# Kernel tuning notes

Measured on AMD Instinct MI355X. Metric: run time of the kernel, lower is better.

Reference implementation:

```python
import jax, jax.numpy as jnp
import numpy as np

B, N, D, H = 2, 192, 256, 8
DH = D // H
SCALE = 1.0 / float(np.sqrt(DH))


def setup_inputs() -> dict:
    key = jax.random.key(0)
    ks = jax.random.split(key, 20)
    def w(k, shape, s=0.02):
        return jax.random.normal(k, shape, dtype=jnp.float32) * s
    inp = {}
    inp['x'] = jax.random.normal(ks[0], (B, N, D), dtype=jnp.float32)
    inp['e'] = jax.random.normal(ks[1], (B, N, N, D), dtype=jnp.float32)
    for name in ['ln_x', 'ln_e', 'ln_x2', 'ln_e2']:
        inp[name + '_g'] = jnp.ones((D,), jnp.float32)
        inp[name + '_b'] = jnp.zeros((D,), jnp.float32)
    # per-head stacked projection weights: [H, D, DH]
    for i, n in enumerate(['Wq_en', 'Wk_en', 'Wv_en', 'Wq_ne', 'Wk_ne', 'Wv_ne']):
        inp[n] = w(ks[2 + i], (H, D, DH))
        inp['b' + n[1:]] = jnp.zeros((H, DH), jnp.float32)
    inp['WOx_w'] = w(ks[10], (D, D)); inp['WOx_b'] = jnp.zeros((D,), jnp.float32)
    inp['WOe_w'] = w(ks[11], (D, D)); inp['WOe_b'] = jnp.zeros((D,), jnp.float32)
    inp['mlpx_w1'] = w(ks[12], (4 * D, D)); inp['mlpx_b1'] = jnp.zeros((4 * D,), jnp.float32)
    inp['mlpx_w2'] = w(ks[13], (D, 4 * D)); inp['mlpx_b2'] = jnp.zeros((D,), jnp.float32)
    inp['mlpe_w1'] = w(ks[14], (4 * D, D)); inp['mlpe_b1'] = jnp.zeros((4 * D,), jnp.float32)
    inp['mlpe_w2'] = w(ks[15], (D, 4 * D)); inp['mlpe_b2'] = jnp.zeros((D,), jnp.float32)
    return inp


def layer_norm(v, g, b, eps=1e-5):
    m = jnp.mean(v, axis=-1, keepdims=True)
    var = jnp.mean((v - m) ** 2, axis=-1, keepdims=True)
    return (v - m) * jax.lax.rsqrt(var + eps) * g + b


def reference(x, e, ln_x_g, ln_x_b, ln_e_g, ln_e_b, ln_x2_g, ln_x2_b, ln_e2_g, ln_e2_b,
              Wq_en, bq_en, Wk_en, bk_en, Wv_en, bv_en,
              Wq_ne, bq_ne, Wk_ne, bk_ne, Wv_ne, bv_ne,
              WOx_w, WOx_b, WOe_w, WOe_b,
              mlpx_w1, mlpx_b1, mlpx_w2, mlpx_b2,
              mlpe_w1, mlpe_b1, mlpe_w2, mlpe_b2):
    b_, n_, d_ = x.shape
    xn = layer_norm(x, ln_x_g, ln_x_b)
    en = layer_norm(e, ln_e_g, ln_e_b)

    # --- edge-to-node cross attention (node i attends over its edges (i, j)) ---
    Q = jnp.einsum('bnd,hde->bnhe', xn, Wq_en) + bq_en          # [B,N,H,DH]
    K = jnp.einsum('bijd,hde->bijhe', en, Wk_en) + bk_en        # [B,N,N,H,DH]
    V = jnp.einsum('bijd,hde->bijhe', en, Wv_en) + bv_en
    s = jnp.einsum('bihe,bijhe->bijh', Q, K) * SCALE            # [B,N,N,H]
    a = jax.nn.softmax(s, axis=2)
    x_heads = jnp.einsum('bijh,bijhe->bihe', a, V)              # [B,N,H,DH]
    x_mha = x_heads.reshape(b_, n_, d_) @ WOx_w.T + WOx_b

    # --- node-to-edge cross attention (edge (i,j) attends over endpoints i, j) ---
    Qe = jnp.einsum('bijd,hde->bijhe', en, Wq_ne) + bq_ne       # [B,N,N,H,DH]
    Kx = jnp.einsum('bnd,hde->bnhe', xn, Wk_ne) + bk_ne         # [B,N,H,DH]
    Vx = jnp.einsum('bnd,hde->bnhe', xn, Wv_ne) + bv_ne
    si = jnp.einsum('bijhe,bihe->bijh', Qe, Kx) * SCALE
    sj = jnp.einsum('bijhe,bjhe->bijh', Qe, Kx) * SCALE
    m = jnp.maximum(si, sj)
    ei = jnp.exp(si - m)
    ej = jnp.exp(sj - m)
    den = ei + ej
    ai = (ei / den)[..., None]                                   # [B,N,N,H,1]
    aj = (ej / den)[..., None]
    e_heads = ai * Vx[:, :, None] + aj * Vx[:, None, :]          # [B,N,N,H,DH]
    e_mha = e_heads.reshape(b_, n_, n_, d_) @ WOe_w.T + WOe_b

    # --- residuals + MLPs ---
    x_out = xn + x_mha
    hx = layer_norm(x_out, ln_x2_g, ln_x2_b)
    hx = jax.nn.leaky_relu(hx @ mlpx_w1.T + mlpx_b1, 0.01) @ mlpx_w2.T + mlpx_b2
    x_out = x_out + hx

    e_out = en + e_mha
    he = layer_norm(e_out, ln_e2_g, ln_e2_b)
    he = jax.nn.leaky_relu(he @ mlpe_w1.T + mlpe_b1, 0.01) @ mlpe_w2.T + mlpe_b2
    e_out = e_out + he
    return (x_out, e_out)
```

## Files before the change

kernel.cpp:

```cpp
#include <hip/hip_runtime.h>
#include <hip/hip_bf16.h>
#include <math.h>

#define BB 2
#define NN 192
#define DD 256
#define HH 8
#define DHH 32
#define SCALE 0.17677669529663687f
#define SJ 4
#define NS6 6
#define NTILE (BB * NN * 6)

typedef __attribute__((ext_vector_type(8))) short short8;
typedef __attribute__((ext_vector_type(4))) float f32x4;


__device__ __forceinline__ float red32(float v) {
    v += __shfl_xor(v, 16);
    v += __shfl_xor(v, 8);
    v += __shfl_xor(v, 4);
    v += __shfl_xor(v, 2);
    v += __shfl_xor(v, 1);
    return v;
}

__device__ __forceinline__ unsigned short f2bf(float f) {
    unsigned int u = __builtin_bit_cast(unsigned int, f);
    u += 0x7FFFu + ((u >> 16) & 1u);
    return (unsigned short)(u >> 16);
}

__device__ __forceinline__ float bf2f(unsigned short u) {
    unsigned int v = ((unsigned int)u) << 16;
    return __builtin_bit_cast(float, v);
}

__device__ __forceinline__ void ln8(float (*xs)[DD], const float* __restrict__ g,
                                    const float* __restrict__ b,
                                    float* mred, float* rred) {
    int t = threadIdx.x;
    int r = t >> 5, l = t & 31;
    float s = 0.f, s2 = 0.f;
#pragma unroll
    for (int u = 0; u < 8; u++) {
        float v = xs[r][l + 32 * u];
        s += v; s2 += v * v;
    }
    s = red32(s); s2 = red32(s2);
    if (l == 0) {
        float mean = s * (1.f / 256.f);
        float var  = s2 * (1.f / 256.f) - mean * mean;
        mred[r] = mean;
        rred[r] = rsqrtf(var + 1e-5f);
    }
    __syncthreads();
    float gt = g[t], bt = b[t];
#pragma unroll
    for (int rr = 0; rr < 8; rr++) {
        float v = xs[rr][t];
        xs[rr][t] = (v - mred[rr]) * rred[rr] * gt + bt;
    }
    __syncthreads();
}

__device__ __forceinline__ void gemm256f8(const unsigned short (*A)[264],
                                          const unsigned short* __restrict__ Wf,
                                          int w, int lane, int fr, int fq,
                                          f32x4 acc[2][2]) {
#pragma unroll
    for (int m = 0; m < 2; m++)
#pragma unroll
        for (int nt = 0; nt < 2; nt++) acc[m][nt] = (f32x4){0.f, 0.f, 0.f, 0.f};
    short8 nb[2];
#pragma unroll
    for (int nt = 0; nt < 2; nt++)
        nb[nt] = *(const short8*)(Wf + (((size_t)(w * 2 + nt) * 8 + 0) * 64 + lane) * 8);
#pragma unroll
    for (int k = 0; k < 8; k++) {
        short8 cb[2];
#pragma unroll
        for (int nt = 0; nt < 2; nt++) cb[nt] = nb[nt];
        if (k < 7) {
#pragma unroll
            for (int nt = 0; nt < 2; nt++)
                nb[nt] = *(const short8*)(Wf + (((size_t)(w * 2 + nt) * 8 + k + 1) * 64 + lane) * 8);
        }
        short8 a0 = *(const short8*)&A[fr][k * 32 + fq * 8];
        short8 a1 = *(const short8*)&A[16 + fr][k * 32 + fq * 8];
#pragma unroll
        for (int nt = 0; nt < 2; nt++) {
            acc[0][nt] = __builtin_amdgcn_mfma_f32_16x16x32_bf16(a0, cb[nt], acc[0][nt], 0, 0, 0);
            acc[1][nt] = __builtin_amdgcn_mfma_f32_16x16x32_bf16(a1, cb[nt], acc[1][nt], 0, 0, 0);
        }
    }
}

__global__ void k_node_prep(const float* __restrict__ x,
                            const float* __restrict__ lnxg, const float* __restrict__ lnxb,
                            const float* __restrict__ Wq, const float* __restrict__ bq,
                            const float* __restrict__ Wk, const float* __restrict__ bk,
                            const float* __restrict__ Wv, const float* __restrict__ bv,
                            float* __restrict__ xn, float* __restrict__ Qb,
                            float* __restrict__ Kx, float* __restrict__ Vx) {
    __shared__ float xs[8][DD];
    __shared__ float mred[8], rred[8];
    int t = threadIdx.x;
    int r0 = blockIdx.x * 8;
    for (int r = 0; r < 8; r++) xs[r][t] = x[(r0 + r) * DD + t];
    __syncthreads();
    ln8(xs, lnxg, lnxb, mred, rred);
    for (int r = 0; r < 8; r++) xn[(r0 + r) * DD + t] = xs[r][t];
    int h = t >> 5, d_ = t & 31;
    const float* wq = Wq + h * DD * DHH + d_;
    const float* wk = Wk + h * DD * DHH + d_;
    const float* wv = Wv + h * DD * DHH + d_;
    float aq[8] = {0}, ak[8] = {0}, av[8] = {0};
    for (int k = 0; k < DD; k++) {
        float w1 = wq[k * DHH], w2 = wk[k * DHH], w3 = wv[k * DHH];
#pragma unroll
        for (int r = 0; r < 8; r++) {
            float e = xs[r][k];
            aq[r] += e * w1; ak[r] += e * w2; av[r] += e * w3;
        }
    }
    float bqt = bq[t], bkt = bk[t], bvt = bv[t];
    for (int r = 0; r < 8; r++) {
        Qb[(r0 + r) * DD + t] = aq[r] + bqt;
        Kx[(r0 + r) * DD + t] = ak[r] + bkt;
        Vx[(r0 + r) * DD + t] = av[r] + bvt;
    }
}

__global__ void k_cvt_all(const float* __restrict__ w1, const float* __restrict__ w2,
                          const float* __restrict__ WOe,
                          const float* __restrict__ Wq, const float* __restrict__ Wk,
                          const float* __restrict__ Wv,
                          unsigned short* __restrict__ w1f, unsigned short* __restrict__ w2f,
                          unsigned short* __restrict__ WOef,
                          unsigned short* __restrict__ Wqf, unsigned short* __restrict__ Wkf,
                          unsigned short* __restrict__ Wvf) {
    int bid = blockIdx.x, t = threadIdx.x;
    short8 out;
    if (bid < 128) {
        int fi = bid * 256 + t;
        int l = fi & 63, g = fi >> 6;
        int fr = l & 15, fq = l >> 4;
        int tau = g >> 3, kap = g & 7;
        const float* src = w1 + (size_t)(tau * 16 + fr) * 256 + kap * 32 + fq * 8;
#pragma unroll
        for (int u = 0; u < 8; u++) out[u] = (short)f2bf(src[u]);
        *(short8*)(w1f + (size_t)fi * 8) = out;
    } else if (bid < 256) {
        int fi = (bid - 128) * 256 + t;
        int l = fi & 63, g = fi >> 6;
        int fr = l & 15, fq = l >> 4;
        int tau = g >> 5, kap = g & 31;
        const float* src = w2 + (size_t)(tau * 16 + fr) * 1024 + kap * 32 + fq * 8;
#pragma unroll
        for (int u = 0; u < 8; u++) out[u] = (short)f2bf(src[u]);
        *(short8*)(w2f + (size_t)fi * 8) = out;
    } else if (bid < 288) {
        int fi = (bid - 256) * 256 + t;
        int l = fi & 63, g = fi >> 6;
        int fr = l & 15, fq = l >> 4;
        int tau = g >> 3, kap = g & 7;
        const float* src = WOe + (size_t)(tau * 16 + fr) * 256 + kap * 32 + fq * 8;
#pragma unroll
        for (int u = 0; u < 8; u++) out[u] = (short)f2bf(src[u]);
        *(short8*)(WOef + (size_t)fi * 8) = out;
    } else {
        int which = (bid - 288) >> 5;
        int fi = ((bid - 288) & 31) * 256 + t;
        int l = fi & 63, g = fi >> 6;
        int fr = l & 15, fq = l >> 4;
        int tau = g >> 3, kap = g & 7;
        int n = tau * 16 + fr;
        int k0 = kap * 32 + fq * 8;
        const float* src = which == 0 ? Wq : which == 1 ? Wk : Wv;
        const float* s2 = src + (size_t)(n >> 5) * 8192 + (n & 31);
#pragma unroll
        for (int u = 0; u < 8; u++) out[u] = (short)f2bf(s2[(size_t)(k0 + u) * 32]);
        unsigned short* dst = which == 0 ? Wqf : which == 1 ? Wkf : Wvf;
        *(short8*)(dst + (size_t)fi * 8) = out;
    }
}

__global__ __launch_bounds__(512, 2) void k_n2e_fused(
    const float* __restrict__ e,
    const float* __restrict__ lneg, const float* __restrict__ lneb,
    const unsigned short* __restrict__ Wqf, const float* __restrict__ bq,
    const unsigned short* __restrict__ Wkf, const float* __restrict__ bk,
    const unsigned short* __restrict__ Wvf, const float* __restrict__ bv,
    const float* __restrict__ Kx, const float* __restrict__ Vx,
    const float* __restrict__ Qb,
    const unsigned short* __restrict__ WOef, const float* __restrict__ WOb,
    const float* __restrict__ ln2g, const float* __restrict__ ln2b,
    const unsigned short* __restrict__ w1f, const float* __restrict__ b1,
    const unsigned short* __restrict__ w2f, const float* __restrict__ b2,
    float* __restrict__ oute,
    float* __restrict__ accP6, float* __restrict__ mP6, float* __restrict__ lP6) {
    __shared__ unsigned short a_bf[32][264];
    __shared__ unsigned short p_bf[32][264];
    __shared__ float KxiS[DD], VxiS[DD], QbS[DD];
    __shared__ float mrow[32], rrow[32];
    __shared__ float sW[32][8], s2W[32][8];
    __shared__ float m2s[32], r2s[32];
    int t = threadIdx.x, lane = t & 63, w = t >> 6;
    int fr = lane & 15, fq = lane >> 4;
    int blk = blockIdx.x;
    int b   = blk / (NN * 6);
    int rem = blk % (NN * 6);
    int i   = rem / 6;
    int spl = rem % 6;
    int j0  = spl * 32;
    int node = b * NN + i;
    size_t ebase = ((size_t)node * NN + j0) * DD;

    {
        int r = t >> 4, sub = t & 15;
        const float4* src4 = (const float4*)(e + ebase + (size_t)r * DD + sub * 16);
        float vals[16];
        float s = 0.f, s2 = 0.f;
#pragma unroll
        for (int u = 0; u < 4; u++) {
            float4 v = src4[u];
            vals[4 * u + 0] = v.x; vals[4 * u + 1] = v.y;
            vals[4 * u + 2] = v.z; vals[4 * u + 3] = v.w;
            s += v.x + v.y + v.z + v.w;
            s2 += v.x * v.x + v.y * v.y + v.z * v.z + v.w * v.w;
        }
        s += __shfl_xor(s, 8); s2 += __shfl_xor(s2, 8);
        s += __shfl_xor(s, 4); s2 += __shfl_xor(s2, 4);
        s += __shfl_xor(s, 2); s2 += __shfl_xor(s2, 2);
        s += __shfl_xor(s, 1); s2 += __shfl_xor(s2, 1);
        float mean = s * (1.f / 256.f);
        float rstd = rsqrtf(s2 * (1.f / 256.f) - mean * mean + 1e-5f);
        if (sub == 0) { mrow[r] = mean; rrow[r] = rstd; }
#pragma unroll
        for (int u = 0; u < 16; u += 2) {
            int col = sub * 16 + u;
            float n0 = (vals[u]     - mean) * rstd * lneg[col]     + lneb[col];
            float n1 = (vals[u + 1] - mean) * rstd * lneg[col + 1] + lneb[col + 1];
            unsigned int pk = (unsigned int)f2bf(n0) | ((unsigned int)f2bf(n1) << 16);
            *(unsigned int*)&a_bf[r][col] = pk;
        }
    }
    if (t < DD) {
        KxiS[t] = Kx[node * DD + t];
        VxiS[t] = Vx[node * DD + t];
        QbS[t]  = Qb[node * DD + t];
    }
    __syncthreads();

    const int nw = w * 32;

    f32x4 accQ[2][2];
    gemm256f8(a_bf, Wqf, w, lane, fr, fq, accQ);
    {
        float bqv[2];
#pragma unroll
        for (int nt = 0; nt < 2; nt++) bqv[nt] = bq[nw + nt * 16 + fr];
#pragma unroll
        for (int m = 0; m < 2; m++)
#pragma unroll
            for (int nt = 0; nt < 2; nt++)
#pragma unroll
                for (int j = 0; j < 4; j++) accQ[m][nt][j] += bqv[nt];
    }

    f32x4 accK[2][2];
    gemm256f8(a_bf, Wkf, w, lane, fr, fq, accK);
#pragma unroll
    for (int nt = 0; nt < 2; nt++) {
        float bb = bk[nw + nt * 16 + fr];
#pragma unroll
        for (int m = 0; m < 2; m++)
#pragma unroll
            for (int j = 0; j < 4; j++) accK[m][nt][j] += bb;
    }

    f32x4 accV[2][2];
    gemm256f8(a_bf, Wvf, w, lane, fr, fq, accV);
#pragma unroll
    for (int nt = 0; nt < 2; nt++) {
        float bb = bv[nw + nt * 16 + fr];
#pragma unroll
        for (int m = 0; m < 2; m++)
#pragma unroll
            for (int j = 0; j < 4; j++) accV[m][nt][j] += bb;
    }

    {
        float QbL[2];
        QbL[0] = QbS[nw + fr];
        QbL[1] = QbS[nw + 16 + fr];
        float p[2][4];
        float mx = -1e30f;
#pragma unroll
        for (int m = 0; m < 2; m++)
#pragma unroll
            for (int j = 0; j < 4; j++) {
                float s = accK[m][0][j] * QbL[0] + accK[m][1][j] * QbL[1];
                s += __shfl_xor(s, 1);
                s += __shfl_xor(s, 2);
                s += __shfl_xor(s, 4);
                s += __shfl_xor(s, 8);
                s *= SCALE;
                p[m][j] = s;
                mx = fmaxf(mx, s);
            }
        mx = fmaxf(mx, __shfl_xor(mx, 16));
        mx = fmaxf(mx, __shfl_xor(mx, 32));
        float lsum = 0.f;
#pragma unroll
        for (int m = 0; m < 2; m++)
#pragma unroll
            for (int j = 0; j < 4; j++) {
                p[m][j] = __expf(p[m][j] - mx);
                lsum += p[m][j];
            }
        lsum += __shfl_xor(lsum, 16);
        lsum += __shfl_xor(lsum, 32);
        float part[2];
#pragma unroll
        for (int nt = 0; nt < 2; nt++) {
            float acc = 0.f;
#pragma unroll
            for (int m = 0; m < 2; m++)
#pragma unroll
                for (int j = 0; j < 4; j++)
                    acc += p[m][j] * accV[m][nt][j];
            acc += __shfl_xor(acc, 16);
            acc += __shfl_xor(acc, 32);
            part[nt] = acc;
        }
        if (fq == 0) {
#pragma unroll
            for (int nt = 0; nt < 2; nt++)
                accP6[((size_t)spl * BB * NN + node) * DD + nw + nt * 16 + fr] = part[nt];
            if (fr == 0) {
                mP6[((size_t)spl * BB * NN + node) * HH + w] = mx;
                lP6[((size_t)spl * BB * NN + node) * HH + w] = lsum;
            }
        }
    }

    float KxiL[2], VxiL[2];
#pragma unroll
    for (int nt = 0; nt < 2; nt++) {
        KxiL[nt] = KxiS[nw + nt * 16 + fr];
        VxiL[nt] = VxiS[nw + nt * 16 + fr];
    }
    float ai[2][4], aj[2][4];
    {
        float Kxj[2][2][4];
#pragma unroll
        for (int m = 0; m < 2; m++)
#pragma unroll
            for (int nt = 0; nt < 2; nt++)
#pragma unroll
                for (int j = 0; j < 4; j++) {
                    int row = m * 16 + fq * 4 + j;
                    Kxj[m][nt][j] = Kx[(size_t)(b * NN + j0 + row) * DD + nw + nt * 16 + fr];
                }
#pragma unroll
        for (int m = 0; m < 2; m++)
#pragma unroll
            for (int j = 0; j < 4; j++) {
                float p = accQ[m][0][j] * KxiL[0] + accQ[m][1][j] * KxiL[1];
                float q = accQ[m][0][j] * Kxj[m][0][j] + accQ[m][1][j] * Kxj[m][1][j];
#pragma unroll
                for (int mk = 1; mk <= 8; mk <<= 1) {
                    p += __shfl_xor(p, mk);
                    q += __shfl_xor(q, mk);
                }
                p *= SCALE; q *= SCALE;
                float mx = fmaxf(p, q);
                float ei = __expf(p - mx), ej = __expf(q - mx);
                float inv = 1.f / (ei + ej);
                ai[m][j] = ei * inv; aj[m][j] = ej * inv;
            }
    }
    {
        float Vxj[2][2][4];
#pragma unroll
        for (int m = 0; m < 2; m++)
#pragma unroll
            for (int nt = 0; nt < 2; nt++)
#pragma unroll
                for (int j = 0; j < 4; j++) {
                    int row = m * 16 + fq * 4 + j;
                    Vxj[m][nt][j] = Vx[(size_t)(b * NN + j0 + row) * DD + nw + nt * 16 + fr];
                }
#pragma unroll
        for (int m = 0; m < 2; m++)
#pragma unroll
            for (int nt = 0; nt < 2; nt++)
#pragma unroll
                for (int j = 0; j < 4; j++) {
                    float v = ai[m][j] * VxiL[nt] + aj[m][j] * Vxj[m][nt][j];
                    p_bf[m * 16 + fq * 4 + j][nw + nt * 16 + fr] = f2bf(v);
                }
    }
    __syncthreads();

    f32x4 accO[2][2];
    gemm256f8(p_bf, WOef, w, lane, fr, fq, accO);

    float epre[2][2][4];
#pragma unroll
    for (int nt = 0; nt < 2; nt++) {
        int col = nw + nt * 16 + fr;
        float bo = WOb[col];
        float gc = lneg[col], bc = lneb[col];
#pragma unroll
        for (int m = 0; m < 2; m++)
#pragma unroll
            for (int j = 0; j < 4; j++) {
                int row = m * 16 + fq * 4 + j;
                float ev = e[ebase + (size_t)row * DD + col];
                float resid = (ev - mrow[row]) * rrow[row] * gc + bc;
                epre[m][nt][j] = resid + accO[m][nt][j] + bo;
            }
    }

#pragma unroll
    for (int m = 0; m < 2; m++)
#pragma unroll
        for (int j = 0; j < 4; j++) {
            float s  = epre[m][0][j] + epre[m][1][j];
            float s2 = epre[m][0][j] * epre[m][0][j] + epre[m][1][j] * epre[m][1][j];
#pragma unroll
            for (int mk = 1; mk <= 8; mk <<= 1) {
                s += __shfl_xor(s, mk);
                s2 += __shfl_xor(s2, mk);
            }
            if (fr == 0) {
                int row = m * 16 + fq * 4 + j;
                sW[row][w] = s;
                s2W[row][w] = s2;
            }
        }
    __syncthreads();
    if (t < 32) {
        float S = 0.f, S2 = 0.f;
#pragma unroll
        for (int ww = 0; ww < 8; ww++) { S += sW[t][ww]; S2 += s2W[t][ww]; }
        float mean = S * (1.f / 256.f);
        float var  = S2 * (1.f / 256.f) - mean * mean;
        m2s[t] = mean;
        r2s[t] = rsqrtf(var + 1e-5f);
    }
    __syncthreads();

#pragma unroll
    for (int nt = 0; nt < 2; nt++) {
        int col = nw + nt * 16 + fr;
        float g2 = ln2g[col], b2c = ln2b[col];
#pragma unroll
        for (int m = 0; m < 2; m++)
#pragma unroll
            for (int j = 0; j < 4; j++) {
                int row = m * 16 + fq * 4 + j;
                p_bf[row][col] = f2bf((epre[m][nt][j] - m2s[row]) * r2s[row] * g2 + b2c);
            }
    }
    __syncthreads();

#define B1ADDR(c, nt, k) (w1f + (((size_t)((c) * 16 + w * 2 + (nt)) * 8 + (k)) * 64 + lane) * 8)
#define B2ADDR(nt, c, k) (w2f + (((size_t)(w * 2 + (nt)) * 32 + (c) * 8 + (k)) * 64 + lane) * 8)
    f32x4 accM[2][2];
#pragma unroll
    for (int m = 0; m < 2; m++)
#pragma unroll
        for (int nt = 0; nt < 2; nt++) accM[m][nt] = (f32x4){0.f, 0.f, 0.f, 0.f};

    for (int c = 0; c < 4; c++) {
        f32x4 acc1[2][2];
#pragma unroll
        for (int m = 0; m < 2; m++)
#pragma unroll
            for (int nt = 0; nt < 2; nt++) acc1[m][nt] = (f32x4){0.f, 0.f, 0.f, 0.f};
        {
            short8 nb[2];
#pragma unroll
            for (int nt = 0; nt < 2; nt++) nb[nt] = *(const short8*)B1ADDR(c, nt, 0);
#pragma unroll
            for (int k = 0; k < 8; k++) {
                short8 cb[2];
#pragma unroll
                for (int nt = 0; nt < 2; nt++) cb[nt] = nb[nt];
                if (k < 7) {
#pragma unroll
                    for (int nt = 0; nt < 2; nt++) nb[nt] = *(const short8*)B1ADDR(c, nt, k + 1);
                }
                short8 a0 = *(const short8*)&p_bf[fr][k * 32 + fq * 8];
                short8 a1 = *(const short8*)&p_bf[16 + fr][k * 32 + fq * 8];
#pragma unroll
                for (int nt = 0; nt < 2; nt++) {
                    acc1[0][nt] = __builtin_amdgcn_mfma_f32_16x16x32_bf16(a0, cb[nt], acc1[0][nt], 0, 0, 0);
                    acc1[1][nt] = __builtin_amdgcn_mfma_f32_16x16x32_bf16(a1, cb[nt], acc1[1][nt], 0, 0, 0);
                }
            }
        }
#pragma unroll
        for (int nt = 0; nt < 2; nt++) {
            int ncol = nw + nt * 16 + fr;
            float bias = b1[c * 256 + ncol];
#pragma unroll
            for (int m = 0; m < 2; m++)
#pragma unroll
                for (int j = 0; j < 4; j++) {
                    float v = acc1[m][nt][j] + bias;
                    v = v > 0.f ? v : 0.01f * v;
                    a_bf[m * 16 + fq * 4 + j][ncol] = f2bf(v);
                }
        }
        __syncthreads();
        {
            short8 nb[2];
#pragma unroll
            for (int nt = 0; nt < 2; nt++) nb[nt] = *(const short8*)B2ADDR(nt, c, 0);
#pragma unroll
            for (int k = 0; k < 8; k++) {
                short8 cb[2];
#pragma unroll
                for (int nt = 0; nt < 2; nt++) cb[nt] = nb[nt];
                if (k < 7) {
#pragma unroll
                    for (int nt = 0; nt < 2; nt++) nb[nt] = *(const short8*)B2ADDR(nt, c, k + 1);
                }
                short8 h0 = *(const short8*)&a_bf[fr][k * 32 + fq * 8];
                short8 h1 = *(const short8*)&a_bf[16 + fr][k * 32 + fq * 8];
#pragma unroll
                for (int nt = 0; nt < 2; nt++) {
                    accM[0][nt] = __builtin_amdgcn_mfma_f32_16x16x32_bf16(h0, cb[nt], accM[0][nt], 0, 0, 0);
                    accM[1][nt] = __builtin_amdgcn_mfma_f32_16x16x32_bf16(h1, cb[nt], accM[1][nt], 0, 0, 0);
                }
            }
        }
        __syncthreads();
    }
#undef B1ADDR
#undef B2ADDR

#pragma unroll
    for (int nt = 0; nt < 2; nt++) {
        int col = nw + nt * 16 + fr;
        float bias = b2[col];
#pragma unroll
        for (int m = 0; m < 2; m++)
#pragma unroll
            for (int j = 0; j < 4; j++) {
                int row = m * 16 + fq * 4 + j;
                oute[ebase + (size_t)row * DD + col] = epre[m][nt][j] + accM[m][nt][j] + bias;
            }
    }
}

__global__ void k_e2n_mergeN(const float* __restrict__ accP, const float* __restrict__ mP,
                             const float* __restrict__ lP, float* __restrict__ xh,
                             int nsplit) {
    int t = threadIdx.x, row = blockIdx.x, h = t >> 5;
    float m = -1e30f;
    for (int s = 0; s < nsplit; s++) m = fmaxf(m, mP[(s * BB * NN + row) * HH + h]);
    float num = 0.f, den = 0.f;
    for (int s = 0; s < nsplit; s++) {
        float c = __expf(mP[(s * BB * NN + row) * HH + h] - m);
        num += accP[((size_t)s * BB * NN + row) * DD + t] * c;
        den += lP[(s * BB * NN + row) * HH + h] * c;
    }
    xh[row * DD + t] = num / den;
}

__global__ void k_x_epi(const float* __restrict__ xh, const float* __restrict__ xn,
                        const float* __restrict__ WO, const float* __restrict__ WOb,
                        const float* __restrict__ ln2g, const float* __restrict__ ln2b,
                        const float* __restrict__ w1, const float* __restrict__ b1,
                        const float* __restrict__ w2, const float* __restrict__ b2,
                        float* __restrict__ outx) {
    __shared__ float hsrc[8][DD];
    __shared__ float xs[8][DD];
    __shared__ float ls[8][DD];
    __shared__ float hh[8][1024];
    __shared__ float mred[8], rred[8];
    int t = threadIdx.x;
    int r0 = blockIdx.x * 8;
    for (int r = 0; r < 8; r++) hsrc[r][t] = xh[(r0 + r) * DD + t];
    __syncthreads();
    float acc[8] = {0};
    const float* wrow = WO + (size_t)t * DD;
    for (int k = 0; k < DD; k++) {
        float w = wrow[k];
#pragma unroll
        for (int r = 0; r < 8; r++) acc[r] += hsrc[r][k] * w;
    }
    float wob = WOb[t];
    for (int r = 0; r < 8; r++) {
        float v = xn[(r0 + r) * DD + t] + acc[r] + wob;
        xs[r][t] = v;
        ls[r][t] = v;
    }
    __syncthreads();
    ln8(ls, ln2g, ln2b, mred, rred);
    for (int p = 0; p < 4; p++) {
        int q = t + p * 256;
        float a2[8] = {0};
        const float* w1r = w1 + (size_t)q * DD;
        for (int k = 0; k < DD; k++) {
            float w = w1r[k];
#pragma unroll
            for (int r = 0; r < 8; r++) a2[r] += ls[r][k] * w;
        }
        float b1q = b1[q];
        for (int r = 0; r < 8; r++) {
            float v = a2[r] + b1q;
            hh[r][q] = v > 0.f ? v : 0.01f * v;
        }
    }
    __syncthreads();
    float a3[8] = {0};
    const float* w2r = w2 + (size_t)t * 1024;
    for (int q = 0; q < 1024; q++) {
        float w = w2r[q];
#pragma unroll
        for (int r = 0; r < 8; r++) a3[r] += hh[r][q] * w;
    }
    float b2t = b2[t];
    for (int r = 0; r < 8; r++)
        outx[(r0 + r) * DD + t] = xs[r][t] + a3[r] + b2t;
}

__global__ void k_e2n_attn(const float* __restrict__ e,
                           const float* __restrict__ lneg, const float* __restrict__ lneb,
                           const float* __restrict__ Wk, const float* __restrict__ bk,
                           const float* __restrict__ Wv, const float* __restrict__ bv,
                           const float* __restrict__ Qb,
                           float* __restrict__ accP, float* __restrict__ mP,
                           float* __restrict__ lP) {
    __shared__ float es[8][DD];
    __shared__ float mred[8], rred[8];
    int t = threadIdx.x;
    int s = blockIdx.x & (SJ - 1);
    int row = blockIdx.x >> 2;
    int h = t >> 5, d_ = t & 31;
    float qt = Qb[row * DD + t];
    float m_s = -1e30f, l_s = 0.f, acc = 0.f;
    const float* wk = Wk + h * DD * DHH + d_;
    const float* wv = Wv + h * DD * DHH + d_;
    float bkt = bk[t], bvt = bv[t];
    for (int j0 = s * (NN / SJ); j0 < (s + 1) * (NN / SJ); j0 += 8) {
        for (int r = 0; r < 8; r++)
            es[r][t] = e[((size_t)row * NN + j0 + r) * DD + t];
        __syncthreads();
        ln8(es, lneg, lneb, mred, rred);
        float aK[8] = {0}, aV[8] = {0};
        for (int k = 0; k < DD; k++) {
            float w1 = wk[k * DHH], w2 = wv[k * DHH];
#pragma unroll
            for (int r = 0; r < 8; r++) {
                float ev = es[r][k];
                aK[r] += ev * w1; aV[r] += ev * w2;
            }
        }
#pragma unroll
        for (int r = 0; r < 8; r++) {
            float sc = red32(qt * (aK[r] + bkt)) * SCALE;
            float vn = aV[r] + bvt;
            float mn = fmaxf(m_s, sc);
            float c = __expf(m_s - mn);
            float p = __expf(sc - mn);
            l_s = l_s * c + p;
            acc = acc * c + p * vn;
            m_s = mn;
        }
        __syncthreads();
    }
    accP[((size_t)s * BB * NN + row) * DD + t] = acc;
    if (d_ == 0) {
        mP[(s * BB * NN + row) * HH + h] = m_s;
        lP[(s * BB * NN + row) * HH + h] = l_s;
    }
}

__global__ void k_n2e(const float* __restrict__ e,
                      const float* __restrict__ lneg, const float* __restrict__ lneb,
                      const float* __restrict__ Wq, const float* __restrict__ bq,
                      const float* __restrict__ Kx, const float* __restrict__ Vx,
                      const float* __restrict__ WO, const float* __restrict__ WOb,
                      float* __restrict__ oute) {
    __shared__ float es[8][DD];
    __shared__ float hs[8][DD];
    __shared__ float mred[8], rred[8];
    int t = threadIdx.x, h = t >> 5, d_ = t & 31;
    int blk = blockIdx.x;
    int b = blk / (NN * (NN / 8));
    int rem = blk % (NN * (NN / 8));
    int i = rem / (NN / 8);
    int j0 = (rem % (NN / 8)) * 8;
    size_t ebase = ((size_t)(b * NN + i) * NN + j0) * DD;
    for (int r = 0; r < 8; r++) es[r][t] = e[ebase + (size_t)r * DD + t];
    __syncthreads();
    ln8(es, lneg, lneb, mred, rred);
    float aQ[8] = {0};
    const float* wq = Wq + h * DD * DHH + d_;
    for (int k = 0; k < DD; k++) {
        float w = wq[k * DHH];
#pragma unroll
        for (int r = 0; r < 8; r++) aQ[r] += es[r][k] * w;
    }
    float bqt = bq[t];
    float kxi = Kx[(b * NN + i) * DD + t];
    float vxi = Vx[(b * NN + i) * DD + t];
#pragma unroll
    for (int r = 0; r < 8; r++) {
        float qe = aQ[r] + bqt;
        float si = red32(qe * kxi) * SCALE;
        float kxj = Kx[(b * NN + j0 + r) * DD + t];
        float sj = red32(qe * kxj) * SCALE;
        float mx = fmaxf(si, sj);
        float ei = __expf(si - mx), ej = __expf(sj - mx);
        float inv = 1.f / (ei + ej);
        float vxj = Vx[(b * NN + j0 + r) * DD + t];
        hs[r][t] = (ei * inv) * vxi + (ej * inv) * vxj;
    }
    __syncthreads();
    float aO[8] = {0};
    const float* wrow = WO + (size_t)t * DD;
    for (int k = 0; k < DD; k++) {
        float w = wrow[k];
#pragma unroll
        for (int r = 0; r < 8; r++) aO[r] += hs[r][k] * w;
    }
    float wob = WOb[t];
    for (int r = 0; r < 8; r++)
        oute[ebase + (size_t)r * DD + t] = es[r][t] + aO[r] + wob;
}

__global__ void k_e_mlp_f32(float* __restrict__ oute,
                            const float* __restrict__ ln2g, const float* __restrict__ ln2b,
                            const float* __restrict__ w1, const float* __restrict__ b1,
                            const float* __restrict__ w2, const float* __restrict__ b2) {
    __shared__ float xs[8][DD];
    __shared__ float ls[8][DD];
    __shared__ float hh[8][1024];
    __shared__ float mred[8], rred[8];
    int t = threadIdx.x;
    size_t r0 = (size_t)blockIdx.x * 8;
    for (int r = 0; r < 8; r++) {
        float v = oute[(r0 + r) * DD + t];
        xs[r][t] = v;
        ls[r][t] = v;
    }
    __syncthreads();
    ln8(ls, ln2g, ln2b, mred, rred);
    for (int p = 0; p < 4; p++) {
        int q = t + p * 256;
        float a2[8] = {0};
        const float* w1r = w1 + (size_t)q * DD;
        for (int k = 0; k < DD; k++) {
            float w = w1r[k];
#pragma unroll
            for (int r = 0; r < 8; r++) a2[r] += ls[r][k] * w;
        }
        float b1q = b1[q];
        for (int r = 0; r < 8; r++) {
            float v = a2[r] + b1q;
            hh[r][q] = v > 0.f ? v : 0.01f * v;
        }
    }
    __syncthreads();
    float a3[8] = {0};
    const float* w2r = w2 + (size_t)t * 1024;
    for (int q = 0; q < 1024; q++) {
        float w = w2r[q];
#pragma unroll
        for (int r = 0; r < 8; r++) a3[r] += hh[r][q] * w;
    }
    float b2t = b2[t];
    for (int r = 0; r < 8; r++)
        oute[(r0 + r) * DD + t] = xs[r][t] + a3[r] + b2t;
}

extern "C" void kernel_launch(void* const* d_in, const int* in_sizes, int n_in,
                              void* d_out, int out_size, void* d_ws, size_t ws_size,
                              hipStream_t stream) {
    (void)in_sizes; (void)n_in; (void)out_size;
    const float* x      = (const float*)d_in[0];
    const float* e      = (const float*)d_in[1];
    const float* ln_x_g = (const float*)d_in[2];
    const float* ln_x_b = (const float*)d_in[3];
    const float* ln_e_g = (const float*)d_in[4];
    const float* ln_e_b = (const float*)d_in[5];
    const float* ln_x2_g = (const float*)d_in[6];
    const float* ln_x2_b = (const float*)d_in[7];
    const float* ln_e2_g = (const float*)d_in[8];
    const float* ln_e2_b = (const float*)d_in[9];
    const float* Wq_en = (const float*)d_in[10];
    const float* bq_en = (const float*)d_in[11];
    const float* Wk_en = (const float*)d_in[12];
    const float* bk_en = (const float*)d_in[13];
    const float* Wv_en = (const float*)d_in[14];
    const float* bv_en = (const float*)d_in[15];
    const float* Wq_ne = (const float*)d_in[16];
    const float* bq_ne = (const float*)d_in[17];
    const float* Wk_ne = (const float*)d_in[18];
    const float* bk_ne = (const float*)d_in[19];
    const float* Wv_ne = (const float*)d_in[20];
    const float* bv_ne = (const float*)d_in[21];
    const float* WOx_w = (const float*)d_in[22];
    const float* WOx_b = (const float*)d_in[23];
    const float* WOe_w = (const float*)d_in[24];
    const float* WOe_b = (const float*)d_in[25];
    const float* mlpx_w1 = (const float*)d_in[26];
    const float* mlpx_b1 = (const float*)d_in[27];
    const float* mlpx_w2 = (const float*)d_in[28];
    const float* mlpx_b2 = (const float*)d_in[29];
    const float* mlpe_w1 = (const float*)d_in[30];
    const float* mlpe_b1 = (const float*)d_in[31];
    const float* mlpe_w2 = (const float*)d_in[32];
    const float* mlpe_b2 = (const float*)d_in[33];

    float* out_x = (float*)d_out;
    float* out_e = out_x + (size_t)BB * NN * DD;

    float* ws = (float*)d_ws;
    float* xn   = ws;
    float* Qb   = xn + 98304;
    float* Kx   = Qb + 98304;
    float* Vx   = Kx + 98304;
    float* xh   = Vx + 98304;
    float* accP = xh + 98304;
    float* mP   = accP + 393216;
    float* lP   = mP + 12288;
    unsigned short* w1f  = (unsigned short*)(lP + 12288);
    unsigned short* w2f  = w1f + 262144;
    unsigned short* WOef = w2f + 262144;
    unsigned short* Wqf  = WOef + 65536;
    unsigned short* Wkf  = Wqf + 65536;
    unsigned short* Wvf  = Wkf + 65536;
    float* accP6 = (float*)(Wvf + 65536);
    float* mP6   = accP6 + 589824;
    float* lP6   = mP6 + 18432;

    const size_t NEED = 909312ull * 4 + 38453504ull * 2;
    bool mfma_path = ws_size >= NEED;

    dim3 blk(256);

    k_node_prep<<<dim3(BB * NN / 8), blk, 0, stream>>>(
        x, ln_x_g, ln_x_b, Wq_en, bq_en, Wk_ne, bk_ne, Wv_ne, bv_ne,
        xn, Qb, Kx, Vx);

    if (mfma_path) {
        k_cvt_all<<<dim3(384), blk, 0, stream>>>(
            mlpe_w1, mlpe_w2, WOe_w, Wq_ne, Wk_en, Wv_en,
            w1f, w2f, WOef, Wqf, Wkf, Wvf);

        k_n2e_fused<<<dim3(NTILE), dim3(512), 0, stream>>>(
            e, ln_e_g, ln_e_b, Wqf, bq_ne, Wkf, bk_en, Wvf, bv_en,
            Kx, Vx, Qb, WOef, WOe_b,
            ln_e2_g, ln_e2_b, w1f, mlpe_b1, w2f, mlpe_b2,
            out_e, accP6, mP6, lP6);

        k_e2n_mergeN<<<dim3(BB * NN), blk, 0, stream>>>(accP6, mP6, lP6, xh, NS6);

        k_x_epi<<<dim3(BB * NN / 8), blk, 0, stream>>>(
            xh, xn, WOx_w, WOx_b, ln_x2_g, ln_x2_b,
            mlpx_w1, mlpx_b1, mlpx_w2, mlpx_b2, out_x);
    } else {
        k_n2e<<<dim3(BB * NN * (NN / 8)), blk, 0, stream>>>(
            e, ln_e_g, ln_e_b, Wq_ne, bq_ne, Kx, Vx, WOe_w, WOe_b, out_e);

        k_e2n_attn<<<dim3(BB * NN * SJ), blk, 0, stream>>>(
            e, ln_e_g, ln_e_b, Wk_en, bk_en, Wv_en, bv_en, Qb, accP, mP, lP);

        k_e2n_mergeN<<<dim3(BB * NN), blk, 0, stream>>>(accP, mP, lP, xh, SJ);

        k_x_epi<<<dim3(BB * NN / 8), blk, 0, stream>>>(
            xh, xn, WOx_w, WOx_b, ln_x2_g, ln_x2_b,
            mlpx_w1, mlpx_b1, mlpx_w2, mlpx_b2, out_x);

        k_e_mlp_f32<<<dim3(BB * NN * NN / 8), blk, 0, stream>>>(
            out_e, ln_e2_g, ln_e2_b, mlpe_w1, mlpe_b1, mlpe_w2, mlpe_b2);
    }
}
```

Measured before the change: 422.6 us.

## Double edge tile rows per block to 64 and reorder Q GEMM after e2n softmax

The fused edge kernel now processes 64 edge rows per block instead of 32, halving the grid and the number of j-splits from six to three. Each wave issues four M-tiles of MFMA per loaded weight fragment, so every global weight load is reused across twice as many rows. The Q projection is also moved after the K/V softmax section to shorten accumulator live ranges. The cost is double the LDS footprint and many more accumulator registers per thread, which may lower occupancy below the declared two blocks per CU or cause spills. Fewer blocks also means less parallelism for the GPU.

```diff
diff --git a/kernel.cpp b/kernel.cpp
--- a/kernel.cpp
+++ b/kernel.cpp
@@ -9,8 +9,8 @@
 #define DHH 32
 #define SCALE 0.17677669529663687f
 #define SJ 4
-#define NS6 6
-#define NTILE (BB * NN * 6)
+#define NS3 3
+#define NTILE3 (BB * NN * 3)
 
 typedef __attribute__((ext_vector_type(8))) short short8;
 typedef __attribute__((ext_vector_type(4))) float f32x4;
@@ -64,12 +64,12 @@
     __syncthreads();
 }
 
-__device__ __forceinline__ void gemm256f8(const unsigned short (*A)[264],
+__device__ __forceinline__ void gemm256m4(const unsigned short (*A)[264],
                                           const unsigned short* __restrict__ Wf,
                                           int w, int lane, int fr, int fq,
-                                          f32x4 acc[2][2]) {
-#pragma unroll
-    for (int m = 0; m < 2; m++)
+                                          f32x4 acc[4][2]) {
+#pragma unroll
+    for (int m = 0; m < 4; m++)
 #pragma unroll
         for (int nt = 0; nt < 2; nt++) acc[m][nt] = (f32x4){0.f, 0.f, 0.f, 0.f};
     short8 nb[2];
@@ -86,13 +86,15 @@
             for (int nt = 0; nt < 2; nt++)
                 nb[nt] = *(const short8*)(Wf + (((size_t)(w * 2 + nt) * 8 + k + 1) * 64 + lane) * 8);
         }
-        short8 a0 = *(const short8*)&A[fr][k * 32 + fq * 8];
-        short8 a1 = *(const short8*)&A[16 + fr][k * 32 + fq * 8];
-#pragma unroll
-        for (int nt = 0; nt < 2; nt++) {
-            acc[0][nt] = __builtin_amdgcn_mfma_f32_16x16x32_bf16(a0, cb[nt], acc[0][nt], 0, 0, 0);
-            acc[1][nt] = __builtin_amdgcn_mfma_f32_16x16x32_bf16(a1, cb[nt], acc[1][nt], 0, 0, 0);
-        }
+        short8 av[4];
+#pragma unroll
+        for (int m = 0; m < 4; m++)
+            av[m] = *(const short8*)&A[m * 16 + fr][k * 32 + fq * 8];
+#pragma unroll
+        for (int nt = 0; nt < 2; nt++)
+#pragma unroll
+            for (int m = 0; m < 4; m++)
+                acc[m][nt] = __builtin_amdgcn_mfma_f32_16x16x32_bf16(av[m], cb[nt], acc[m][nt], 0, 0, 0);
     }
 }
 
@@ -199,38 +201,37 @@
     const unsigned short* __restrict__ w1f, const float* __restrict__ b1,
     const unsigned short* __restrict__ w2f, const float* __restrict__ b2,
     float* __restrict__ oute,
-    float* __restrict__ accP6, float* __restrict__ mP6, float* __restrict__ lP6) {
-    __shared__ unsigned short a_bf[32][264];
-    __shared__ unsigned short p_bf[32][264];
+    float* __restrict__ accP3, float* __restrict__ mP3, float* __restrict__ lP3) {
+    __shared__ unsigned short a_bf[64][264];
+    __shared__ unsigned short p_bf[64][264];
     __shared__ float KxiS[DD], VxiS[DD], QbS[DD];
-    __shared__ float mrow[32], rrow[32];
-    __shared__ float sW[32][8], s2W[32][8];
-    __shared__ float m2s[32], r2s[32];
+    __shared__ float mrow[64], rrow[64];
+    __shared__ float sW[64][8], s2W[64][8];
+    __shared__ float m2s[64], r2s[64];
     int t = threadIdx.x, lane = t & 63, w = t >> 6;
     int fr = lane & 15, fq = lane >> 4;
     int blk = blockIdx.x;
-    int b   = blk / (NN * 6);
-    int rem = blk % (NN * 6);
-    int i   = rem / 6;
-    int spl = rem % 6;
-    int j0  = spl * 32;
+    int b   = blk / (NN * 3);
+    int rem = blk % (NN * 3);
+    int i   = rem / 3;
+    int spl = rem % 3;
+    int j0  = spl * 64;
     int node = b * NN + i;
     size_t ebase = ((size_t)node * NN + j0) * DD;
 
     {
-        int r = t >> 4, sub = t & 15;
-        const float4* src4 = (const float4*)(e + ebase + (size_t)r * DD + sub * 16);
-        float vals[16];
+        int r = t >> 3, sub = t & 7;
+        const float4* src4 = (const float4*)(e + ebase + (size_t)r * DD + sub * 32);
+        float vals[32];
         float s = 0.f, s2 = 0.f;
 #pragma unroll
-        for (int u = 0; u < 4; u++) {
+        for (int u = 0; u < 8; u++) {
             float4 v = src4[u];
             vals[4 * u + 0] = v.x; vals[4 * u + 1] = v.y;
             vals[4 * u + 2] = v.z; vals[4 * u + 3] = v.w;
             s += v.x + v.y + v.z + v.w;
             s2 += v.x * v.x + v.y * v.y + v.z * v.z + v.w * v.w;
         }
-        s += __shfl_xor(s, 8); s2 += __shfl_xor(s2, 8);
         s += __shfl_xor(s, 4); s2 += __shfl_xor(s2, 4);
         s += __shfl_xor(s, 2); s2 += __shfl_xor(s2, 2);
         s += __shfl_xor(s, 1); s2 += __shfl_xor(s2, 1);
@@ -238,8 +239,8 @@
         float rstd = rsqrtf(s2 * (1.f / 256.f) - mean * mean + 1e-5f);
         if (sub == 0) { mrow[r] = mean; rrow[r] = rstd; }
 #pragma unroll
-        for (int u = 0; u < 16; u += 2) {
-            int col = sub * 16 + u;
+        for (int u = 0; u < 32; u += 2) {
+            int col = sub * 32 + u;
             float n0 = (vals[u]     - mean) * rstd * lneg[col]     + lneb[col];
             float n1 = (vals[u + 1] - mean) * rstd * lneg[col + 1] + lneb[col + 1];
             unsigned int pk = (unsigned int)f2bf(n0) | ((unsigned int)f2bf(n1) << 16);
@@ -255,38 +256,24 @@
 
     const int nw = w * 32;
 
-    f32x4 accQ[2][2];
-    gemm256f8(a_bf, Wqf, w, lane, fr, fq, accQ);
-    {
-        float bqv[2];
-#pragma unroll
-        for (int nt = 0; nt < 2; nt++) bqv[nt] = bq[nw + nt * 16 + fr];
-#pragma unroll
-        for (int m = 0; m < 2; m++)
-#pragma unroll
-            for (int nt = 0; nt < 2; nt++)
-#pragma unroll
-                for (int j = 0; j < 4; j++) accQ[m][nt][j] += bqv[nt];
-    }
-
-    f32x4 accK[2][2];
-    gemm256f8(a_bf, Wkf, w, lane, fr, fq, accK);
+    f32x4 accK[4][2];
+    gemm256m4(a_bf, Wkf, w, lane, fr, fq, accK);
 #pragma unroll
     for (int nt = 0; nt < 2; nt++) {
         float bb = bk[nw + nt * 16 + fr];
 #pragma unroll
-        for (int m = 0; m < 2; m++)
+        for (int m = 0; m < 4; m++)
 #pragma unroll
             for (int j = 0; j < 4; j++) accK[m][nt][j] += bb;
     }
 
-    f32x4 accV[2][2];
-    gemm256f8(a_bf, Wvf, w, lane, fr, fq, accV);
+    f32x4 accV[4][2];
+    gemm256m4(a_bf, Wvf, w, lane, fr, fq, accV);
 #pragma unroll
     for (int nt = 0; nt < 2; nt++) {
         float bb = bv[nw + nt * 16 + fr];
 #pragma unroll
-        for (int m = 0; m < 2; m++)
+        for (int m = 0; m < 4; m++)
 #pragma unroll
             for (int j = 0; j < 4; j++) accV[m][nt][j] += bb;
     }
@@ -295,10 +282,10 @@
         float QbL[2];
         QbL[0] = QbS[nw + fr];
         QbL[1] = QbS[nw + 16 + fr];
-        float p[2][4];
+        float p[4][4];
         float mx = -1e30f;
 #pragma unroll
-        for (int m = 0; m < 2; m++)
+        for (int m = 0; m < 4; m++)
 #pragma unroll
             for (int j = 0; j < 4; j++) {
                 float s = accK[m][0][j] * QbL[0] + accK[m][1][j] * QbL[1];
@@ -314,7 +301,7 @@
         mx = fmaxf(mx, __shfl_xor(mx, 32));
         float lsum = 0.f;
 #pragma unroll
-        for (int m = 0; m < 2; m++)
+        for (int m = 0; m < 4; m++)
 #pragma unroll
             for (int j = 0; j < 4; j++) {
                 p[m][j] = __expf(p[m][j] - mx);
@@ -327,7 +314,7 @@
         for (int nt = 0; nt < 2; nt++) {
             float acc = 0.f;
 #pragma unroll
-            for (int m = 0; m < 2; m++)
+            for (int m = 0; m < 4; m++)
 #pragma unroll
                 for (int j = 0; j < 4; j++)
                     acc += p[m][j] * accV[m][nt][j];
@@ -338,12 +325,26 @@
         if (fq == 0) {
 #pragma unroll
             for (int nt = 0; nt < 2; nt++)
-                accP6[((size_t)spl * BB * NN + node) * DD + nw + nt * 16 + fr] = part[nt];
+                accP3[((size_t)spl * BB * NN + node) * DD + nw + nt * 16 + fr] = part[nt];
             if (fr == 0) {
-                mP6[((size_t)spl * BB * NN + node) * HH + w] = mx;
-                lP6[((size_t)spl * BB * NN + node) * HH + w] = lsum;
-            }
-        }
+                mP3[((size_t)spl * BB * NN + node) * HH + w] = mx;
+                lP3[((size_t)spl * BB * NN + node) * HH + w] = lsum;
+            }
+        }
+    }
+
+    f32x4 accQ[4][2];
+    gemm256m4(a_bf, Wqf, w, lane, fr, fq, accQ);
+    {
+        float bqv[2];
+#pragma unroll
+        for (int nt = 0; nt < 2; nt++) bqv[nt] = bq[nw + nt * 16 + fr];
+#pragma unroll
+        for (int m = 0; m < 4; m++)
+#pragma unroll
+            for (int nt = 0; nt < 2; nt++)
+#pragma unroll
+                for (int j = 0; j < 4; j++) accQ[m][nt][j] += bqv[nt];
     }
 
     float KxiL[2], VxiL[2];
@@ -352,70 +353,50 @@
         KxiL[nt] = KxiS[nw + nt * 16 + fr];
         VxiL[nt] = VxiS[nw + nt * 16 + fr];
     }
-    float ai[2][4], aj[2][4];
-    {
-        float Kxj[2][2][4];
-#pragma unroll
-        for (int m = 0; m < 2; m++)
-#pragma unroll
-            for (int nt = 0; nt < 2; nt++)
-#pragma unroll
-                for (int j = 0; j < 4; j++) {
-                    int row = m * 16 + fq * 4 + j;
-                    Kxj[m][nt][j] = Kx[(size_t)(b * NN + j0 + row) * DD + nw + nt * 16 + fr];
-                }
-#pragma unroll
-        for (int m = 0; m < 2; m++)
-#pragma unroll
-            for (int j = 0; j < 4; j++) {
-                float p = accQ[m][0][j] * KxiL[0] + accQ[m][1][j] * KxiL[1];
-                float q = accQ[m][0][j] * Kxj[m][0][j] + accQ[m][1][j] * Kxj[m][1][j];
-#pragma unroll
-                for (int mk = 1; mk <= 8; mk <<= 1) {
-                    p += __shfl_xor(p, mk);
-                    q += __shfl_xor(q, mk);
-                }
-                p *= SCALE; q *= SCALE;
-                float mx = fmaxf(p, q);
-                float ei = __expf(p - mx), ej = __expf(q - mx);
-                float inv = 1.f / (ei + ej);
-                ai[m][j] = ei * inv; aj[m][j] = ej * inv;
-            }
-    }
-    {
-        float Vxj[2][2][4];
-#pragma unroll
-        for (int m = 0; m < 2; m++)
-#pragma unroll
-            for (int nt = 0; nt < 2; nt++)
-#pragma unroll
-                for (int j = 0; j < 4; j++) {
-                    int row = m * 16 + fq * 4 + j;
-                    Vxj[m][nt][j] = Vx[(size_t)(b * NN + j0 + row) * DD + nw + nt * 16 + fr];
-                }
-#pragma unroll
-        for (int m = 0; m < 2; m++)
-#pragma unroll
-            for (int nt = 0; nt < 2; nt++)
-#pragma unroll
-                for (int j = 0; j < 4; j++) {
-                    float v = ai[m][j] * VxiL[nt] + aj[m][j] * Vxj[m][nt][j];
-                    p_bf[m * 16 + fq * 4 + j][nw + nt * 16 + fr] = f2bf(v);
-                }
-    }
-    __syncthreads();
-
-    f32x4 accO[2][2];
-    gemm256f8(p_bf, WOef, w, lane, fr, fq, accO);
-
-    float epre[2][2][4];
+    float ai[4][4], aj[4][4];
+#pragma unroll
+    for (int m = 0; m < 4; m++)
+#pragma unroll
+        for (int j = 0; j < 4; j++) {
+            int row = m * 16 + fq * 4 + j;
+            float k0v = Kx[(size_t)(b * NN + j0 + row) * DD + nw + fr];
+            float k1v = Kx[(size_t)(b * NN + j0 + row) * DD + nw + 16 + fr];
+            float p = accQ[m][0][j] * KxiL[0] + accQ[m][1][j] * KxiL[1];
+            float q = accQ[m][0][j] * k0v + accQ[m][1][j] * k1v;
+#pragma unroll
+            for (int mk = 1; mk <= 8; mk <<= 1) {
+                p += __shfl_xor(p, mk);
+                q += __shfl_xor(q, mk);
+            }
+            p *= SCALE; q *= SCALE;
+            float mx = fmaxf(p, q);
+            float ei = __expf(p - mx), ej = __expf(q - mx);
+            float inv = 1.f / (ei + ej);
+            ai[m][j] = ei * inv; aj[m][j] = ej * inv;
+        }
+#pragma unroll
+    for (int m = 0; m < 4; m++)
+#pragma unroll
+        for (int j = 0; j < 4; j++) {
+            int row = m * 16 + fq * 4 + j;
+            float v0 = Vx[(size_t)(b * NN + j0 + row) * DD + nw + fr];
+            float v1 = Vx[(size_t)(b * NN + j0 + row) * DD + nw + 16 + fr];
+            p_bf[row][nw + fr]      = f2bf(ai[m][j] * VxiL[0] + aj[m][j] * v0);
+            p_bf[row][nw + 16 + fr] = f2bf(ai[m][j] * VxiL[1] + aj[m][j] * v1);
+        }
+    __syncthreads();
+
+    f32x4 accO[4][2];
+    gemm256m4(p_bf, WOef, w, lane, fr, fq, accO);
+
+    float epre[4][2][4];
 #pragma unroll
     for (int nt = 0; nt < 2; nt++) {
         int col = nw + nt * 16 + fr;
         float bo = WOb[col];
         float gc = lneg[col], bc = lneb[col];
 #pragma unroll
-        for (int m = 0; m < 2; m++)
+        for (int m = 0; m < 4; m++)
 #pragma unroll
             for (int j = 0; j < 4; j++) {
                 int row = m * 16 + fq * 4 + j;
@@ -426,7 +407,7 @@
     }
 
 #pragma unroll
-    for (int m = 0; m < 2; m++)
+    for (int m = 0; m < 4; m++)
 #pragma unroll
         for (int j = 0; j < 4; j++) {
             float s  = epre[m][0][j] + epre[m][1][j];
@@ -443,7 +424,7 @@
             }
         }
     __syncthreads();
-    if (t < 32) {
+    if (t < 64) {
         float S = 0.f, S2 = 0.f;
 #pragma unroll
         for (int ww = 0; ww < 8; ww++) { S += sW[t][ww]; S2 += s2W[t][ww]; }
@@ -459,7 +440,7 @@
         int col = nw + nt * 16 + fr;
         float g2 = ln2g[col], b2c = ln2b[col];
 #pragma unroll
-        for (int m = 0; m < 2; m++)
+        for (int m = 0; m < 4; m++)
 #pragma unroll
             for (int j = 0; j < 4; j++) {
                 int row = m * 16 + fq * 4 + j;
@@ -470,16 +451,16 @@
 
 #define B1ADDR(c, nt, k) (w1f + (((size_t)((c) * 16 + w * 2 + (nt)) * 8 + (k)) * 64 + lane) * 8)
 #define B2ADDR(nt, c, k) (w2f + (((size_t)(w * 2 + (nt)) * 32 + (c) * 8 + (k)) * 64 + lane) * 8)
-    f32x4 accM[2][2];
-#pragma unroll
-    for (int m = 0; m < 2; m++)
+    f32x4 accM[4][2];
+#pragma unroll
+    for (int m = 0; m < 4; m++)
 #pragma unroll
         for (int nt = 0; nt < 2; nt++) accM[m][nt] = (f32x4){0.f, 0.f, 0.f, 0.f};
 
     for (int c = 0; c < 4; c++) {
-        f32x4 acc1[2][2];
-#pragma unroll
-        for (int m = 0; m < 2; m++)
+        f32x4 acc1[4][2];
+#pragma unroll
+        for (int m = 0; m < 4; m++)
 #pragma unroll
             for (int nt = 0; nt < 2; nt++) acc1[m][nt] = (f32x4){0.f, 0.f, 0.f, 0.f};
         {
@@ -495,13 +476,15 @@
 #pragma unroll
                     for (int nt = 0; nt < 2; nt++) nb[nt] = *(const short8*)B1ADDR(c, nt, k + 1);
                 }
-                short8 a0 = *(const short8*)&p_bf[fr][k * 32 + fq * 8];
-                short8 a1 = *(const short8*)&p_bf[16 + fr][k * 32 + fq * 8];
-#pragma unroll
-                for (int nt = 0; nt < 2; nt++) {
-                    acc1[0][nt] = __builtin_amdgcn_mfma_f32_16x16x32_bf16(a0, cb[nt], acc1[0][nt], 0, 0, 0);
-                    acc1[1][nt] = __builtin_amdgcn_mfma_f32_16x16x32_bf16(a1, cb[nt], acc1[1][nt], 0, 0, 0);
-                }
+                short8 av[4];
+#pragma unroll
+                for (int m = 0; m < 4; m++)
+                    av[m] = *(const short8*)&p_bf[m * 16 + fr][k * 32 + fq * 8];
+#pragma unroll
+                for (int nt = 0; nt < 2; nt++)
+#pragma unroll
+                    for (int m = 0; m < 4; m++)
+                        acc1[m][nt] = __builtin_amdgcn_mfma_f32_16x16x32_bf16(av[m], cb[nt], acc1[m][nt], 0, 0, 0);
             }
         }
 #pragma unroll
@@ -509,7 +492,7 @@
             int ncol = nw + nt * 16 + fr;
             float bias = b1[c * 256 + ncol];
 #pragma unroll
-            for (int m = 0; m < 2; m++)
+            for (int m = 0; m < 4; m++)
 #pragma unroll
                 for (int j = 0; j < 4; j++) {
                     float v = acc1[m][nt][j] + bias;
@@ -531,13 +514,15 @@
 #pragma unroll
                     for (int nt = 0; nt < 2; nt++) nb[nt] = *(const short8*)B2ADDR(nt, c, k + 1);
                 }
-                short8 h0 = *(const short8*)&a_bf[fr][k * 32 + fq * 8];
-                short8 h1 = *(const short8*)&a_bf[16 + fr][k * 32 + fq * 8];
-#pragma unroll
-                for (int nt = 0; nt < 2; nt++) {
-                    accM[0][nt] = __builtin_amdgcn_mfma_f32_16x16x32_bf16(h0, cb[nt], accM[0][nt], 0, 0, 0);
-                    accM[1][nt] = __builtin_amdgcn_mfma_f32_16x16x32_bf16(h1, cb[nt], accM[1][nt], 0, 0, 0);
-                }
+                short8 hv[4];
+#pragma unroll
+                for (int m = 0; m < 4; m++)
+                    hv[m] = *(const short8*)&a_bf[m * 16 + fr][k * 32 + fq * 8];
+#pragma unroll
+                for (int nt = 0; nt < 2; nt++)
+#pragma unroll
+                    for (int m = 0; m < 4; m++)
+                        accM[m][nt] = __builtin_amdgcn_mfma_f32_16x16x32_bf16(hv[m], cb[nt], accM[m][nt], 0, 0, 0);
             }
         }
         __syncthreads();
@@ -550,7 +535,7 @@
         int col = nw + nt * 16 + fr;
         float bias = b2[col];
 #pragma unroll
-        for (int m = 0; m < 2; m++)
+        for (int m = 0; m < 4; m++)
 #pragma unroll
             for (int j = 0; j < 4; j++) {
                 int row = m * 16 + fq * 4 + j;
@@ -840,9 +825,9 @@
     unsigned short* Wqf  = WOef + 65536;
     unsigned short* Wkf  = Wqf + 65536;
     unsigned short* Wvf  = Wkf + 65536;
-    float* accP6 = (float*)(Wvf + 65536);
-    float* mP6   = accP6 + 589824;
-    float* lP6   = mP6 + 18432;
+    float* accP3 = (float*)(Wvf + 65536);
+    float* mP3   = accP3 + 294912;
+    float* lP3   = mP3 + 9216;
 
     const size_t NEED = 909312ull * 4 + 38453504ull * 2;
     bool mfma_path = ws_size >= NEED;
@@ -858,13 +843,13 @@
             mlpe_w1, mlpe_w2, WOe_w, Wq_ne, Wk_en, Wv_en,
             w1f, w2f, WOef, Wqf, Wkf, Wvf);
 
-        k_n2e_fused<<<dim3(NTILE), dim3(512), 0, stream>>>(
+        k_n2e_fused<<<dim3(NTILE3), dim3(512), 0, stream>>>(
             e, ln_e_g, ln_e_b, Wqf, bq_ne, Wkf, bk_en, Wvf, bv_en,
             Kx, Vx, Qb, WOef, WOe_b,
             ln_e2_g, ln_e2_b, w1f, mlpe_b1, w2f, mlpe_b2,
-            out_e, accP6, mP6, lP6);
-
-        k_e2n_mergeN<<<dim3(BB * NN), blk, 0, stream>>>(accP6, mP6, lP6, xh, NS6);
+            out_e, accP3, mP3, lP3);
+
+        k_e2n_mergeN<<<dim3(BB * NN), blk, 0, stream>>>(accP3, mP3, lP3, xh, NS3);
 
         k_x_epi<<<dim3(BB * NN / 8), blk, 0, stream>>>(
             xh, xn, WOx_w, WOx_b, ln_x2_g, ln_x2_b,
```

Result: faster. 396.4 us (-6.2%).
